# Kernel tuning notes

Hardware: AMD Instinct MI355X
Metric: run time of the kernel (lower is better)

## Reference

```python
import jax, jax.numpy as jnp
import numpy as np


def setup_inputs() -> dict:
    key = jax.random.key(0)
    k1, k2, k3 = jax.random.split(key, 3)
    B, L, D = 2, 8192, 1024
    x = jax.random.normal(k1, (B, L, D), dtype=jnp.float32)
    h = jax.random.normal(k2, (L, D), dtype=jnp.float32)
    bias = jax.random.normal(k3, (D,), dtype=jnp.float32) * 0.02
    return {"x": x, "h": h, "bias": bias}


def reference(x, h, bias):
    # x: (B, L, D), h: (filter_len, D), bias: (D,)
    B, L, D = x.shape
    filter_len = h.shape[0]
    # next power of two >= L + filter_len - 1 (static, from shapes)
    fft_size = 1 << int(L + filter_len - 1).bit_length()
    x_f = jnp.fft.rfft(x, n=fft_size, axis=1)          # (B, fft_size//2+1, D) complex
    h_f = jnp.fft.rfft(h, n=fft_size, axis=0)          # (fft_size//2+1, D) complex
    y = jnp.fft.irfft(x_f * h_f[None, :, :], n=fft_size, axis=1)
    y = y[:, :L, :]                                    # causal-length truncation
    return y + bias
```

## Files before the change

kernel.cpp:

```cpp
#include <hip/hip_runtime.h>

#define D_CH   1024
#define L_SEQ  8192
#define W_N    3.8349519697141029e-4f
#define W128A  4.90873852123405e-2f

__device__ __forceinline__ unsigned f2bf(float v){
  union { float f; unsigned u; } x; x.f = v;
  unsigned r = x.u + 0x7fffu + ((x.u >> 16) & 1u);
  return r >> 16;
}
__device__ __forceinline__ float bf2f(unsigned v){
  union { float f; unsigned u; } x; x.u = v << 16;
  return x.f;
}
__device__ __forceinline__ unsigned packc(float r, float i){
  return f2bf(r) | (f2bf(i) << 16);
}
__device__ __forceinline__ float2 upk(unsigned u){
  return make_float2(bf2f(u & 0xffffu), bf2f(u >> 16));
}

__device__ __host__ constexpr int bitrev4(int j){
  return ((j&1)<<3)|((j&2)<<1)|((j&4)>>1)|((j&8)>>3);
}
__device__ __host__ constexpr int bitrev3(int j){
  return ((j&1)<<2)|(j&2)|((j&4)>>2);
}

template<int SGN>
__device__ __forceinline__ void dft16(float2* x){
  const float TC[8] = {1.f, 0.9238795325f, 0.7071067812f, 0.3826834324f,
                       0.f, -0.3826834324f, -0.7071067812f, -0.9238795325f};
  const float TS[8] = {0.f, -0.3826834324f, -0.7071067812f, -0.9238795325f,
                       -1.f, -0.9238795325f, -0.7071067812f, -0.3826834324f};
#pragma unroll
  for (int len = 16; len >= 2; len >>= 1){
    const int half = len >> 1, tstep = 16 / len;
#pragma unroll
    for (int st = 0; st < 16; st += len){
#pragma unroll
      for (int j = 0; j < half; j++){
        const float wr = TC[j*tstep];
        const float wi = (SGN > 0) ? TS[j*tstep] : -TS[j*tstep];
        const int a = st + j, b = a + half;
        const float ur = x[a].x, ui = x[a].y;
        const float vr = x[b].x, vi = x[b].y;
        x[a].x = ur + vr; x[a].y = ui + vi;
        const float dr = ur - vr, di = ui - vi;
        x[b].x = dr*wr - di*wi;
        x[b].y = dr*wi + di*wr;
      }
    }
  }
}

template<int SGN>
__device__ __forceinline__ void dft8(float2* x){
  const float TC[4] = {1.f, 0.7071067812f, 0.f, -0.7071067812f};
  const float TS[4] = {0.f, -0.7071067812f, -1.f, -0.7071067812f};
#pragma unroll
  for (int len = 8; len >= 2; len >>= 1){
    const int half = len >> 1, tstep = 8 / len;
#pragma unroll
    for (int st = 0; st < 8; st += len){
#pragma unroll
      for (int j = 0; j < half; j++){
        const float wr = TC[j*tstep];
        const float wi = (SGN > 0) ? TS[j*tstep] : -TS[j*tstep];
        const int a = st + j, b = a + half;
        const float ur = x[a].x, ui = x[a].y;
        const float vr = x[b].x, vi = x[b].y;
        x[a].x = ur + vr; x[a].y = ui + vi;
        const float dr = ur - vr, di = ui - vi;
        x[b].x = dr*wr - di*wi;
        x[b].y = dr*wi + di*wr;
      }
    }
  }
}

template<int SGN>
__device__ __forceinline__ void fft128(float2* v, float2* lds, int lane, int p){
  dft16<SGN>(v);
#pragma unroll
  for (int slot = 0; slot < 8; slot++){
    const int r = bitrev3(slot);
    float sn, cs;
    __sincosf(-(float)SGN * W128A * (float)(p*(2*r)), &sn, &cs);
    const float2 a = v[slot];
    lds[(p*8 + r)*64 + lane] = make_float2(a.x*cs - a.y*sn, a.x*sn + a.y*cs);
  }
  __syncthreads();
  float2 t8[8];
#pragma unroll
  for (int pp = 0; pp < 8; pp++) t8[pp] = lds[(pp*8 + p)*64 + lane];
  dft8<SGN>(t8);
#pragma unroll
  for (int t = 0; t < 8; t++) v[t] = t8[t];
  __syncthreads();
#pragma unroll
  for (int slot = 8; slot < 16; slot++){
    const int r = bitrev3(slot - 8);
    float sn, cs;
    __sincosf(-(float)SGN * W128A * (float)(p*(2*r+1)), &sn, &cs);
    const float2 a = v[slot];
    lds[(p*8 + r)*64 + lane] = make_float2(a.x*cs - a.y*sn, a.x*sn + a.y*cs);
  }
  __syncthreads();
#pragma unroll
  for (int pp = 0; pp < 8; pp++) t8[pp] = lds[(pp*8 + p)*64 + lane];
  dft8<SGN>(t8);
#pragma unroll
  for (int t = 0; t < 8; t++) v[8 + t] = t8[t];
}

__global__ __launch_bounds__(512, 8)
void k1_step1(const float* __restrict__ x, const float* __restrict__ h,
              unsigned* __restrict__ Az, unsigned* __restrict__ Ah){
  __shared__ float2 lds[4096];
  const int n2 = blockIdx.x, dg = blockIdx.y, mode = blockIdx.z;
  const int lane = threadIdx.x & 63, p = threadIdx.x >> 6;
  const int d = dg*64 + lane;

  float2 v[16];
  if (mode == 0){
    const float* x0 = x;
    const float* x1 = x + (size_t)L_SEQ * D_CH;
#pragma unroll
    for (int q = 0; q < 8; q++){
      const size_t off = (size_t)(n2 + 128*(p + 8*q)) * D_CH + d;
      v[q] = make_float2(x0[off], x1[off]);
    }
  } else {
#pragma unroll
    for (int q = 0; q < 8; q++){
      const size_t off = (size_t)(n2 + 128*(p + 8*q)) * D_CH + d;
      v[q] = make_float2(h[off], 0.0f);
    }
  }
#pragma unroll
  for (int q = 8; q < 16; q++) v[q] = make_float2(0.f, 0.f);

  fft128<1>(v, lds, lane, p);

  unsigned* __restrict__ A = mode ? Ah : Az;
#pragma unroll
  for (int c = 0; c < 2; c++){
#pragma unroll
    for (int t = 0; t < 8; t++){
      const int k1v = (2*p + c) + 16*bitrev3(t);
      float sn, cs;
      __sincosf(-W_N * (float)(k1v * n2), &sn, &cs);
      const float2 a = v[c*8 + t];
      A[((size_t)k1v*128 + n2)*D_CH + d] =
        packc(a.x*cs - a.y*sn, a.x*sn + a.y*cs);
    }
  }
}

__global__ __launch_bounds__(512, 4)
void k2_zh(unsigned* __restrict__ Az, const unsigned* __restrict__ Ah){
  __shared__ float2 lds[4096];
  const int k1 = blockIdx.x, dg = blockIdx.y;
  const int lane = threadIdx.x & 63, p = threadIdx.x >> 6;
  const int d = dg*64 + lane;
  const size_t base = (size_t)k1 * 128 * D_CH + d;

  unsigned ha[16], za[16];
#pragma unroll
  for (int q = 0; q < 16; q++)
    ha[q] = Ah[base + (size_t)(p + 8*q) * D_CH];
#pragma unroll
  for (int q = 0; q < 16; q++)
    za[q] = Az[base + (size_t)(p + 8*q) * D_CH];

  float2 v[16];
#pragma unroll
  for (int q = 0; q < 16; q++) v[q] = upk(ha[q]);
  fft128<1>(v, lds, lane, p);
  unsigned hs[16];
  const float sc = 1.0f / 16384.0f;
#pragma unroll
  for (int i = 0; i < 16; i++) hs[i] = packc(v[i].x * sc, v[i].y * sc);
  __syncthreads();

#pragma unroll
  for (int q = 0; q < 16; q++) v[q] = upk(za[q]);
  fft128<1>(v, lds, lane, p);

#pragma unroll
  for (int i = 0; i < 16; i++){
    const float2 hv = upk(hs[i]);
    const float zr = v[i].x, zi = v[i].y;
    v[i] = make_float2(zr*hv.x - zi*hv.y, zr*hv.y + zi*hv.x);
  }

  __syncthreads();
  float2 w[16];
#pragma unroll
  for (int c = 0; c < 2; c++)
#pragma unroll
    for (int t = 0; t < 8; t += 2){
      const int k2 = (2*p + c) + 16*bitrev3(t);
      lds[k2*64 + lane] = v[c*8 + t];
    }
  __syncthreads();
#pragma unroll
  for (int q = 0; q < 8; q++) w[q] = lds[(p + 8*q)*64 + lane];
  __syncthreads();
#pragma unroll
  for (int c = 0; c < 2; c++)
#pragma unroll
    for (int t = 1; t < 8; t += 2){
      const int k2 = (2*p + c) + 16*bitrev3(t) - 64;
      lds[k2*64 + lane] = v[c*8 + t];
    }
  __syncthreads();
#pragma unroll
  for (int q = 0; q < 8; q++) w[8 + q] = lds[(p + 8*q)*64 + lane];
  __syncthreads();
#pragma unroll
  for (int q = 0; q < 16; q++) v[q] = w[q];

  fft128<-1>(v, lds, lane, p);

#pragma unroll
  for (int c = 0; c < 2; c++){
#pragma unroll
    for (int t = 0; t < 8; t++){
      const int m2 = (2*p + c) + 16*bitrev3(t);
      const float2 a = v[c*8 + t];
      Az[base + (size_t)m2 * D_CH] = packc(a.x, a.y);
    }
  }
}

__global__ __launch_bounds__(512, 6)
void k3_inv2(const unsigned* __restrict__ Bz, const float* __restrict__ bias,
             float* __restrict__ out){
  __shared__ float2 lds[4096];
  const int m2 = blockIdx.x, dg = blockIdx.y;
  const int lane = threadIdx.x & 63, p = threadIdx.x >> 6;
  const int d = dg*64 + lane;
  const float bv = bias[d];

  unsigned raw[16];
#pragma unroll
  for (int q = 0; q < 16; q++){
    const int k1 = p + 8*q;
    raw[q] = Bz[((size_t)k1*128 + m2) * D_CH + d];
  }
  float2 v[16];
#pragma unroll
  for (int q = 0; q < 16; q++){
    const int k1 = p + 8*q;
    float sn, cs;
    __sincosf(W_N * (float)(m2 * k1), &sn, &cs);
    const float2 a = upk(raw[q]);
    v[q] = make_float2(a.x*cs - a.y*sn, a.x*sn + a.y*cs);
  }

  fft128<-1>(v, lds, lane, p);

#pragma unroll
  for (int c = 0; c < 2; c++){
#pragma unroll
    for (int t = 0; t < 8; t += 2){
      const int m1 = (2*p + c) + 16*bitrev3(t);
      const int tseq = m2 + 128*m1;
      const float2 a = v[c*8 + t];
      out[(size_t)tseq * D_CH + d]            = a.x + bv;
      out[(size_t)(L_SEQ + tseq) * D_CH + d]  = a.y + bv;
    }
  }
}

extern "C" void kernel_launch(void* const* d_in, const int* in_sizes, int n_in,
                              void* d_out, int out_size, void* d_ws, size_t ws_size,
                              hipStream_t stream){
  (void)in_sizes; (void)n_in; (void)out_size;
  const float* x    = (const float*)d_in[0];
  const float* h    = (const float*)d_in[1];
  const float* bias = (const float*)d_in[2];
  float* out = (float*)d_out;

  const size_t REGION = (size_t)128 * 128 * D_CH * sizeof(unsigned);
  unsigned *r1, *r2;
  if (ws_size >= 2 * REGION){
    r1 = (unsigned*)d_ws;
    r2 = (unsigned*)((char*)d_ws + REGION);
  } else {
    r1 = (unsigned*)d_out;
    r2 = (unsigned*)d_ws;
  }

  const dim3 blk(512, 1, 1);
  hipLaunchKernelGGL(k1_step1, dim3(128,16,2), blk, 0, stream, x, h, r1, r2);
  hipLaunchKernelGGL(k2_zh,    dim3(128,16,1), blk, 0, stream, r1, r2);
  hipLaunchKernelGGL(k3_inv2,  dim3(128,16,1), blk, 0, stream, r1, bias, out);
}
```

Baseline: 245.3 us.

## Replace per-element sincos twiddles with recurrences and add DIT reverse FFT

```diff
diff --git a/kernel.cpp b/kernel.cpp
--- a/kernel.cpp
+++ b/kernel.cpp
@@ -5,6 +5,10 @@
 #define W_N    3.8349519697141029e-4f
 #define W128A  4.90873852123405e-2f
 
+#ifndef __has_builtin
+#define __has_builtin(x) 0
+#endif
+
 __device__ __forceinline__ unsigned f2bf(float v){
   union { float f; unsigned u; } x; x.f = v;
   unsigned r = x.u + 0x7fffu + ((x.u >> 16) & 1u);
@@ -14,11 +18,21 @@
   union { float f; unsigned u; } x; x.u = v << 16;
   return x.f;
 }
+#if __has_builtin(__builtin_amdgcn_cvt_pk_bf16_f32)
+__device__ __forceinline__ unsigned packc(float r, float i){
+  auto h = __builtin_amdgcn_cvt_pk_bf16_f32(r, i);
+  unsigned u; __builtin_memcpy(&u, &h, 4); return u;
+}
+#else
 __device__ __forceinline__ unsigned packc(float r, float i){
   return f2bf(r) | (f2bf(i) << 16);
 }
+#endif
 __device__ __forceinline__ float2 upk(unsigned u){
   return make_float2(bf2f(u & 0xffffu), bf2f(u >> 16));
+}
+__device__ __forceinline__ float2 cmul(float2 a, float2 b){
+  return make_float2(a.x*b.x - a.y*b.y, a.x*b.y + a.y*b.x);
 }
 
 __device__ __host__ constexpr int bitrev4(int j){
@@ -81,15 +95,42 @@
 }
 
 template<int SGN>
+__device__ __forceinline__ void dft8_dit(float2* x){
+  const float TC[4] = {1.f, 0.7071067812f, 0.f, -0.7071067812f};
+  const float TS[4] = {0.f, -0.7071067812f, -1.f, -0.7071067812f};
+#pragma unroll
+  for (int len = 2; len <= 8; len <<= 1){
+    const int half = len >> 1, tstep = 8 / len;
+#pragma unroll
+    for (int st = 0; st < 8; st += len){
+#pragma unroll
+      for (int j = 0; j < half; j++){
+        const float wr = TC[j*tstep];
+        const float wi = (SGN > 0) ? TS[j*tstep] : -TS[j*tstep];
+        const int a = st + j, b = a + half;
+        const float br = x[b].x, bi = x[b].y;
+        const float tr = br*wr - bi*wi, ti = br*wi + bi*wr;
+        const float ar = x[a].x, ai = x[a].y;
+        x[a].x = ar + tr; x[a].y = ai + ti;
+        x[b].x = ar - tr; x[b].y = ai - ti;
+      }
+    }
+  }
+}
+
+template<int SGN>
 __device__ __forceinline__ void fft128(float2* v, float2* lds, int lane, int p){
   dft16<SGN>(v);
-#pragma unroll
-  for (int slot = 0; slot < 8; slot++){
-    const int r = bitrev3(slot);
-    float sn, cs;
-    __sincosf(-(float)SGN * W128A * (float)(p*(2*r)), &sn, &cs);
-    const float2 a = v[slot];
-    lds[(p*8 + r)*64 + lane] = make_float2(a.x*cs - a.y*sn, a.x*sn + a.y*cs);
+  float sn, cs;
+  __sincosf(-(float)SGN * W128A * (float)p, &sn, &cs);
+  const float2 base  = make_float2(cs, sn);
+  const float2 base2 = cmul(base, base);
+  float2 w = make_float2(1.f, 0.f);
+#pragma unroll
+  for (int r = 0; r < 8; r++){
+    const int slot = bitrev3(r);
+    lds[(p*8 + r)*64 + lane] = cmul(v[slot], w);
+    w = cmul(w, base2);
   }
   __syncthreads();
   float2 t8[8];
@@ -99,13 +140,12 @@
 #pragma unroll
   for (int t = 0; t < 8; t++) v[t] = t8[t];
   __syncthreads();
-#pragma unroll
-  for (int slot = 8; slot < 16; slot++){
-    const int r = bitrev3(slot - 8);
-    float sn, cs;
-    __sincosf(-(float)SGN * W128A * (float)(p*(2*r+1)), &sn, &cs);
-    const float2 a = v[slot];
-    lds[(p*8 + r)*64 + lane] = make_float2(a.x*cs - a.y*sn, a.x*sn + a.y*cs);
+  w = base;
+#pragma unroll
+  for (int r = 0; r < 8; r++){
+    const int slot = 8 + bitrev3(r);
+    lds[(p*8 + r)*64 + lane] = cmul(v[slot], w);
+    w = cmul(w, base2);
   }
   __syncthreads();
 #pragma unroll
@@ -115,7 +155,54 @@
   for (int t = 0; t < 8; t++) v[8 + t] = t8[t];
 }
 
-__global__ __launch_bounds__(512, 8)
+template<int SGN>
+__device__ __forceinline__ void fft128_rev(float2* v, float2* lds, int lane, int p){
+  float2 B[16];
+#pragma unroll
+  for (int c = 0; c < 2; c++){
+    float2 t8[8];
+#pragma unroll
+    for (int t = 0; t < 8; t++) t8[t] = v[c*8 + t];
+    dft8_dit<SGN>(t8);
+    const int s = 2*p + c;
+    float sn, cs;
+    __sincosf(-(float)SGN * W128A * (float)s, &sn, &cs);
+    const float2 bs = make_float2(cs, sn);
+    float2 w = make_float2(1.f, 0.f);
+#pragma unroll
+    for (int u = 0; u < 8; u++){
+      B[c*8 + u] = cmul(t8[u], w);
+      w = cmul(w, bs);
+    }
+  }
+#pragma unroll
+  for (int c = 0; c < 2; c++)
+#pragma unroll
+    for (int u = 0; u < 4; u++)
+      lds[(u*16 + 2*p + c)*64 + lane] = B[c*8 + u];
+  __syncthreads();
+  float2 g[16];
+  if (p < 4){
+#pragma unroll
+    for (int s = 0; s < 16; s++) g[s] = lds[(p*16 + s)*64 + lane];
+  }
+  __syncthreads();
+#pragma unroll
+  for (int c = 0; c < 2; c++)
+#pragma unroll
+    for (int u = 4; u < 8; u++)
+      lds[((u-4)*16 + 2*p + c)*64 + lane] = B[c*8 + u];
+  __syncthreads();
+  if (p >= 4){
+#pragma unroll
+    for (int s = 0; s < 16; s++) g[s] = lds[((p-4)*16 + s)*64 + lane];
+  }
+  dft16<SGN>(g);
+#pragma unroll
+  for (int t = 0; t < 16; t++) v[t] = g[t];
+}
+
+__global__ __launch_bounds__(512, 4)
 void k1_step1(const float* __restrict__ x, const float* __restrict__ h,
               unsigned* __restrict__ Az, unsigned* __restrict__ Ah){
   __shared__ float2 lds[4096];
@@ -144,18 +231,31 @@
 
   fft128<1>(v, lds, lane, p);
 
+  float sn, cs;
+  __sincosf(-W_N * (float)(2*p*n2), &sn, &cs);
+  float2 b0 = make_float2(cs, sn);
+  __sincosf(-W_N * (float)n2, &sn, &cs);
+  const float2 u1 = make_float2(cs, sn);
+  float2 b1 = cmul(b0, u1);
+  __sincosf(-W_N * (float)(16*n2), &sn, &cs);
+  const float2 s16 = make_float2(cs, sn);
+
   unsigned* __restrict__ A = mode ? Ah : Az;
 #pragma unroll
-  for (int c = 0; c < 2; c++){
-#pragma unroll
-    for (int t = 0; t < 8; t++){
-      const int k1v = (2*p + c) + 16*bitrev3(t);
-      float sn, cs;
-      __sincosf(-W_N * (float)(k1v * n2), &sn, &cs);
-      const float2 a = v[c*8 + t];
-      A[((size_t)k1v*128 + n2)*D_CH + d] =
-        packc(a.x*cs - a.y*sn, a.x*sn + a.y*cs);
-    }
+  for (int r = 0; r < 8; r++){
+    const int t = bitrev3(r);
+    {
+      const int k1v = 2*p + 16*r;
+      const float2 a = cmul(v[t], b0);
+      A[((size_t)k1v*128 + n2)*D_CH + d] = packc(a.x, a.y);
+    }
+    {
+      const int k1v = 2*p + 1 + 16*r;
+      const float2 a = cmul(v[8 + t], b1);
+      A[((size_t)k1v*128 + n2)*D_CH + d] = packc(a.x, a.y);
+    }
+    b0 = cmul(b0, s16);
+    b1 = cmul(b1, s16);
   }
 }
 
@@ -197,46 +297,17 @@
   }
 
   __syncthreads();
-  float2 w[16];
-#pragma unroll
-  for (int c = 0; c < 2; c++)
-#pragma unroll
-    for (int t = 0; t < 8; t += 2){
-      const int k2 = (2*p + c) + 16*bitrev3(t);
-      lds[k2*64 + lane] = v[c*8 + t];
-    }
-  __syncthreads();
-#pragma unroll
-  for (int q = 0; q < 8; q++) w[q] = lds[(p + 8*q)*64 + lane];
-  __syncthreads();
-#pragma unroll
-  for (int c = 0; c < 2; c++)
-#pragma unroll
-    for (int t = 1; t < 8; t += 2){
-      const int k2 = (2*p + c) + 16*bitrev3(t) - 64;
-      lds[k2*64 + lane] = v[c*8 + t];
-    }
-  __syncthreads();
-#pragma unroll
-  for (int q = 0; q < 8; q++) w[8 + q] = lds[(p + 8*q)*64 + lane];
-  __syncthreads();
-#pragma unroll
-  for (int q = 0; q < 16; q++) v[q] = w[q];
-
-  fft128<-1>(v, lds, lane, p);
-
-#pragma unroll
-  for (int c = 0; c < 2; c++){
-#pragma unroll
-    for (int t = 0; t < 8; t++){
-      const int m2 = (2*p + c) + 16*bitrev3(t);
-      const float2 a = v[c*8 + t];
-      Az[base + (size_t)m2 * D_CH] = packc(a.x, a.y);
-    }
-  }
-}
-
-__global__ __launch_bounds__(512, 6)
+  fft128_rev<-1>(v, lds, lane, p);
+
+#pragma unroll
+  for (int t = 0; t < 16; t++){
+    const int m2 = p + 8*bitrev4(t);
+    const float2 a = v[t];
+    Az[base + (size_t)m2 * D_CH] = packc(a.x, a.y);
+  }
+}
+
+__global__ __launch_bounds__(512, 4)
 void k3_inv2(const unsigned* __restrict__ Bz, const float* __restrict__ bias,
              float* __restrict__ out){
   __shared__ float2 lds[4096];
@@ -251,14 +322,16 @@
     const int k1 = p + 8*q;
     raw[q] = Bz[((size_t)k1*128 + m2) * D_CH + d];
   }
+  float sn, cs;
+  __sincosf(W_N * (float)(m2*p), &sn, &cs);
+  float2 b = make_float2(cs, sn);
+  __sincosf(W_N * (float)(8*m2), &sn, &cs);
+  const float2 st8 = make_float2(cs, sn);
   float2 v[16];
 #pragma unroll
   for (int q = 0; q < 16; q++){
-    const int k1 = p + 8*q;
-    float sn, cs;
-    __sincosf(W_N * (float)(m2 * k1), &sn, &cs);
-    const float2 a = upk(raw[q]);
-    v[q] = make_float2(a.x*cs - a.y*sn, a.x*sn + a.y*cs);
+    v[q] = cmul(upk(raw[q]), b);
+    b = cmul(b, st8);
   }
 
   fft128<-1>(v, lds, lane, p);
```

Result: no change. 247.3 us (+0.8%).
